# Kernel tuning notes

Measured on AMD Instinct MI355X. Metric: run time of the kernel, lower is better.

## Reference

```python
import jax, jax.numpy as jnp
import numpy as np

NEG_SLOPE = 0.01  # torch leaky_relu default

N_NODES = 100000
N_EDGES = 1600000
D = 64
N_BBOX = 4096


def setup_inputs() -> dict:
    key = jax.random.key(0)
    ks = jax.random.split(key, 9)
    x = jax.random.normal(ks[0], (N_NODES, D), dtype=jnp.float32)
    edge_index = jax.random.randint(ks[1], (2, N_EDGES), 0, N_NODES, dtype=jnp.int64)
    bbox = jax.random.randint(ks[2], (N_BBOX,), 0, N_NODES, dtype=jnp.int64)
    s = 1.0 / np.sqrt(D)
    W1_rel = jax.random.normal(ks[3], (D, D), dtype=jnp.float32) * s
    b1 = jax.random.normal(ks[4], (D,), dtype=jnp.float32) * s
    W1_root = jax.random.normal(ks[5], (D, D), dtype=jnp.float32) * s
    W2_rel = jax.random.normal(ks[6], (D, D), dtype=jnp.float32) * s
    b2 = jax.random.normal(ks[7], (D,), dtype=jnp.float32) * s
    W2_root = jax.random.normal(ks[8], (D, D), dtype=jnp.float32) * s
    return {"x": x, "edge_index": edge_index, "bbox": bbox,
            "W1_rel": W1_rel, "b1": b1, "W1_root": W1_root,
            "W2_rel": W2_rel, "b2": b2, "W2_root": W2_root}


def graph_conv(x, src, dst, W_rel, b, W_root):
    # PyG GraphConv: out_i = W_rel @ (sum_{j in N(i)} x_j) + b + W_root @ x_i
    msg = x[src]                                        # [E, D] gather
    agg = jax.ops.segment_sum(msg, dst, num_segments=x.shape[0])  # [N, D] scatter-add
    return agg @ W_rel + b + x @ W_root


def reference(x, edge_index, bbox, W1_rel, b1, W1_root, W2_rel, b2, W2_root):
    src, dst = edge_index[0], edge_index[1]
    h = graph_conv(x, src, dst, W1_rel, b1, W1_root)
    h = jax.nn.leaky_relu(h, NEG_SLOPE)
    # dropout is identity at inference (training=False)
    h = graph_conv(h, src, dst, W2_rel, b2, W2_root)
    h = jax.nn.leaky_relu(h, NEG_SLOPE)
    return h[bbox]
```

## Files before the change

### kernel.cpp

```cpp
#include <hip/hip_runtime.h>

#define N_NODES 100000
#define N_EDGES 1600000
#define D 64
#define N_BBOX 4096
#define CAP 64
#define NBITW 3136

typedef short bf16x8 __attribute__((ext_vector_type(8)));
typedef float f32x4 __attribute__((ext_vector_type(4)));

__device__ __forceinline__ float readlane_f(float v, int l) {
  return __int_as_float(__builtin_amdgcn_readlane(__float_as_int(v), l));
}
__device__ __forceinline__ int bperm(int srclane, int v) {
  return __builtin_amdgcn_ds_bpermute(srclane << 2, v);
}
__device__ __forceinline__ float lrelu(float v) {
  return fmaxf(v, 0.01f * v);
}
__device__ __forceinline__ bool testbit(const unsigned* bits, int i) {
  return (bits[i >> 5] >> (i & 31)) & 1u;
}
__device__ __forceinline__ short f2bf(float f) {
  unsigned u = __float_as_uint(f);
  u += 0x7FFFu + ((u >> 16) & 1u);
  return (short)(u >> 16);
}
__device__ __forceinline__ bf16x8 pack_bf8(float4 lo, float4 hi) {
  bf16x8 r;
  r[0] = f2bf(lo.x); r[1] = f2bf(lo.y); r[2] = f2bf(lo.z); r[3] = f2bf(lo.w);
  r[4] = f2bf(hi.x); r[5] = f2bf(hi.y); r[6] = f2bf(hi.z); r[7] = f2bf(hi.w);
  return r;
}

__global__ __launch_bounds__(256) void mark_kernel(const int* __restrict__ bbox,
                                                   unsigned* __restrict__ is_bbox_bits,
                                                   unsigned* __restrict__ needed_bits) {
  int t = blockIdx.x * blockDim.x + threadIdx.x;
  if (t < N_BBOX) {
    int n = bbox[t];
    unsigned m = 1u << (n & 31);
    atomicOr(&is_bbox_bits[n >> 5], m);
    atomicOr(&needed_bits[n >> 5], m);
  }
}

__global__ __launch_bounds__(256) void mark_needed_kernel(
    const int* __restrict__ src, const int* __restrict__ dst,
    const unsigned* __restrict__ is_bbox_bits, unsigned* __restrict__ needed_bits) {
  int e = blockIdx.x * blockDim.x + threadIdx.x;
  if (e >= N_EDGES) return;
  int d = dst[e];
  if (testbit(is_bbox_bits, d)) {
    int s = src[e];
    atomicOr(&needed_bits[s >> 5], 1u << (s & 31));
  }
}

__global__ __launch_bounds__(256) void fill_kernel(const int* __restrict__ src,
                                                   const int* __restrict__ dst,
                                                   const unsigned* __restrict__ needed_bits,
                                                   int* __restrict__ cnt,
                                                   int* __restrict__ slots) {
  int e = blockIdx.x * blockDim.x + threadIdx.x;
  if (e >= N_EDGES) return;
  int d = dst[e];
  if (!testbit(needed_bits, d)) return;
  int p = atomicAdd(&cnt[d], 1);
  if (p < CAP) slots[(size_t)d * CAP + p] = src[e];
}

__global__ __launch_bounds__(256) void gather1_kernel(const float4* __restrict__ x4,
                                                      const unsigned* __restrict__ needed_bits,
                                                      const int* __restrict__ cnt,
                                                      const int* __restrict__ slots,
                                                      float4* __restrict__ agg4) {
  const int wid = (blockIdx.x * blockDim.x + threadIdx.x) >> 6;
  if (wid >= N_NODES) return;
  if (!testbit(needed_bits, wid)) return;
  const int lane = threadIdx.x & 63;
  const int g = lane >> 4, c = lane & 15;

  int n = cnt[wid];
  n = (n > CAP) ? CAP : n;
  const int myslot = (lane < n) ? slots[(size_t)wid * CAP + lane] : 0;

  float4 acc = make_float4(0.f, 0.f, 0.f, 0.f);
  for (int e0 = 0; e0 < n; e0 += 32) {
    int idx[8], s[8];
    float4 v[8];
#pragma unroll
    for (int u = 0; u < 8; u++) {
      idx[u] = e0 + u * 4 + g;
      s[u] = bperm(idx[u], myslot);
    }
#pragma unroll
    for (int u = 0; u < 8; u++) {
      v[u] = make_float4(0.f, 0.f, 0.f, 0.f);
      if (idx[u] < n) v[u] = x4[(size_t)s[u] * 16 + c];
    }
#pragma unroll
    for (int u = 0; u < 8; u++) {
      acc.x += v[u].x; acc.y += v[u].y; acc.z += v[u].z; acc.w += v[u].w;
    }
  }
  acc.x += __shfl_xor(acc.x, 16); acc.y += __shfl_xor(acc.y, 16);
  acc.z += __shfl_xor(acc.z, 16); acc.w += __shfl_xor(acc.w, 16);
  acc.x += __shfl_xor(acc.x, 32); acc.y += __shfl_xor(acc.y, 32);
  acc.z += __shfl_xor(acc.z, 32); acc.w += __shfl_xor(acc.w, 32);
  if (g == 0) agg4[(size_t)wid * 16 + c] = acc;
}

__global__ __launch_bounds__(256, 1) void dense1_mfma_kernel(
    const float* __restrict__ x, const float* __restrict__ W1rel,
    const float* __restrict__ b1, const float* __restrict__ W1root,
    float* __restrict__ hbuf) {
  const int lane = threadIdx.x & 63;
  const int cn = lane & 15;
  const int quad = lane >> 4;
  const int wid0 = (blockIdx.x * blockDim.x + threadIdx.x) >> 6;
  const int nwaves = (gridDim.x * blockDim.x) >> 6;

  bf16x8 brel[2][4], broot[2][4];
#pragma unroll
  for (int kh = 0; kh < 2; kh++)
#pragma unroll
    for (int nt = 0; nt < 4; nt++)
#pragma unroll
      for (int i = 0; i < 8; i++) {
        const int k = kh * 32 + quad * 8 + i;
        brel[kh][nt][i] = f2bf(W1rel[k * D + nt * 16 + cn]);
        broot[kh][nt][i] = f2bf(W1root[k * D + nt * 16 + cn]);
      }
  float bj[4];
#pragma unroll
  for (int nt = 0; nt < 4; nt++) bj[nt] = b1[nt * 16 + cn];

  for (int tile = wid0; tile < N_NODES / 16; tile += nwaves) {
    const int node0 = tile * 16;
    const float* arow = hbuf + (size_t)(node0 + cn) * D;
    const float* xrow = x + (size_t)(node0 + cn) * D;

    f32x4 acc[4] = {};
#pragma unroll
    for (int kh = 0; kh < 2; kh++) {
      const int kb = kh * 32 + quad * 8;
      const float4 fa0 = *(const float4*)(arow + kb);
      const float4 fa1 = *(const float4*)(arow + kb + 4);
      const float4 fx0 = *(const float4*)(xrow + kb);
      const float4 fx1 = *(const float4*)(xrow + kb + 4);
      const bf16x8 a_agg = pack_bf8(fa0, fa1);
      const bf16x8 a_x = pack_bf8(fx0, fx1);
#pragma unroll
      for (int nt = 0; nt < 4; nt++) {
        acc[nt] = __builtin_amdgcn_mfma_f32_16x16x32_bf16(a_agg, brel[kh][nt],
                                                          acc[nt], 0, 0, 0);
        acc[nt] = __builtin_amdgcn_mfma_f32_16x16x32_bf16(a_x, broot[kh][nt],
                                                          acc[nt], 0, 0, 0);
      }
    }
#pragma unroll
    for (int nt = 0; nt < 4; nt++) {
#pragma unroll
      for (int r = 0; r < 4; r++) {
        const int row = quad * 4 + r;
        hbuf[(size_t)(node0 + row) * D + nt * 16 + cn] = lrelu(acc[nt][r] + bj[nt]);
      }
    }
  }
}

__global__ __launch_bounds__(256, 1) void layer2_kernel(
    const float4* __restrict__ h4, const int* __restrict__ cnt,
    const int* __restrict__ slots, const int* __restrict__ bbox,
    const float* __restrict__ W2rel, const float* __restrict__ b2,
    const float* __restrict__ W2root, float* __restrict__ out) {
  const int t = (blockIdx.x * blockDim.x + threadIdx.x) >> 6;
  if (t >= N_BBOX) return;
  const int lane = threadIdx.x & 63;
  const int g = lane >> 4, c = lane & 15;

  float wrel[D], wroot[D];
#pragma unroll
  for (int k = 0; k < D; k++) {
    wrel[k] = W2rel[k * D + lane];
    wroot[k] = W2root[k * D + lane];
  }
  const float bj = b2[lane];

  const int node = __builtin_amdgcn_readfirstlane(bbox[t]);
  int n = cnt[node];
  n = (n > CAP) ? CAP : n;
  const int myslot = (lane < n) ? slots[(size_t)node * CAP + lane] : 0;

  float4 acc = make_float4(0.f, 0.f, 0.f, 0.f);
  for (int e0 = 0; e0 < n; e0 += 32) {
    int idx[8], s[8];
    float4 v[8];
#pragma unroll
    for (int u = 0; u < 8; u++) {
      idx[u] = e0 + u * 4 + g;
      s[u] = bperm(idx[u], myslot);
    }
#pragma unroll
    for (int u = 0; u < 8; u++) {
      v[u] = make_float4(0.f, 0.f, 0.f, 0.f);
      if (idx[u] < n) v[u] = h4[(size_t)s[u] * 16 + c];
    }
#pragma unroll
    for (int u = 0; u < 8; u++) {
      acc.x += v[u].x; acc.y += v[u].y; acc.z += v[u].z; acc.w += v[u].w;
    }
  }
  acc.x += __shfl_xor(acc.x, 16); acc.y += __shfl_xor(acc.y, 16);
  acc.z += __shfl_xor(acc.z, 16); acc.w += __shfl_xor(acc.w, 16);
  acc.x += __shfl_xor(acc.x, 32); acc.y += __shfl_xor(acc.y, 32);
  acc.z += __shfl_xor(acc.z, 32); acc.w += __shfl_xor(acc.w, 32);

  const float hi = ((const float*)h4)[(size_t)node * D + lane];
  float s0 = 0.f, s1 = 0.f, s2 = 0.f, s3 = 0.f;
#pragma unroll
  for (int k = 0; k < D; k += 2) {
    const float a0 = (k & 2) ? readlane_f(acc.z, k >> 2) : readlane_f(acc.x, k >> 2);
    const float a1 = ((k + 1) & 2) ? readlane_f(acc.w, (k + 1) >> 2)
                                   : readlane_f(acc.y, (k + 1) >> 2);
    s0 += a0 * wrel[k];
    s1 += readlane_f(hi, k) * wroot[k];
    s2 += a1 * wrel[k + 1];
    s3 += readlane_f(hi, k + 1) * wroot[k + 1];
  }
  out[(size_t)t * D + lane] = lrelu(bj + ((s0 + s1) + (s2 + s3)));
}


extern "C" void kernel_launch(void* const* d_in, const int* in_sizes, int n_in,
                              void* d_out, int out_size, void* d_ws, size_t ws_size,
                              hipStream_t stream) {
  const float* x = (const float*)d_in[0];
  const int* ei = (const int*)d_in[1];
  const int* src = ei;
  const int* dst = ei + N_EDGES;
  const int* bbox = (const int*)d_in[2];
  const float* W1rel = (const float*)d_in[3];
  const float* b1 = (const float*)d_in[4];
  const float* W1root = (const float*)d_in[5];
  const float* W2rel = (const float*)d_in[6];
  const float* b2 = (const float*)d_in[7];
  const float* W2root = (const float*)d_in[8];
  float* out = (float*)d_out;

  char* ws = (char*)d_ws;
  size_t off = 0;
  auto alloc = [&](size_t bytes) -> char* {
    char* p = ws + off;
    off = (off + bytes + 511) & ~(size_t)511;
    return p;
  };
  unsigned* is_bbox_bits = (unsigned*)alloc(NBITW * sizeof(unsigned));
  unsigned* needed_bits = (unsigned*)alloc(NBITW * sizeof(unsigned));
  int* cnt = (int*)alloc(N_NODES * sizeof(int));
  char* zero_end = ws + off;
  int* slots = (int*)alloc((size_t)N_NODES * CAP * sizeof(int));
  float* hbuf = (float*)alloc((size_t)N_NODES * D * sizeof(float));

  hipMemsetAsync(is_bbox_bits, 0, (size_t)(zero_end - (char*)is_bbox_bits), stream);
  mark_kernel<<<(N_BBOX + 255) / 256, 256, 0, stream>>>(bbox, is_bbox_bits,
                                                        needed_bits);
  mark_needed_kernel<<<(N_EDGES + 255) / 256, 256, 0, stream>>>(
      src, dst, is_bbox_bits, needed_bits);
  fill_kernel<<<(N_EDGES + 255) / 256, 256, 0, stream>>>(src, dst, needed_bits,
                                                         cnt, slots);
  gather1_kernel<<<(N_NODES + 3) / 4, 256, 0, stream>>>(
      (const float4*)x, needed_bits, cnt, slots, (float4*)hbuf);
  dense1_mfma_kernel<<<512, 256, 0, stream>>>(x, W1rel, b1, W1root, hbuf);
  layer2_kernel<<<(N_BBOX + 3) / 4, 256, 0, stream>>>(
      (const float4*)hbuf, cnt, slots, bbox, W2rel, b2, W2root, out);
}
```

Measured before the change: 201.7 us.

## Fuse layer-1 gather and dense MFMA through LDS, skip unneeded nodes

Merges the neighbor-aggregation kernel and the dense MFMA kernel into one kernel. Each block aggregates 64 nodes into LDS, then runs bf16 MFMA directly from LDS, so the aggregate no longer round-trips through global memory. hbuf is now written only for nodes layer 2 needs. A small prep kernel pre-transposes and converts the weights to bf16 so each block loads them with vector reads instead of converting scalars itself. The risks are lower occupancy from launch_bounds(256,1) plus LDS use, and serialized per-wave gather loops of 16 nodes each.

```diff
diff --git a/kernel.cpp b/kernel.cpp
--- a/kernel.cpp
+++ b/kernel.cpp
@@ -6,6 +6,7 @@
 #define N_BBOX 4096
 #define CAP 64
 #define NBITW 3136
+#define NTILE 1563
 
 typedef short bf16x8 __attribute__((ext_vector_type(8)));
 typedef float f32x4 __attribute__((ext_vector_type(4)));
@@ -71,102 +72,107 @@
   if (p < CAP) slots[(size_t)d * CAP + p] = src[e];
 }
 
-__global__ __launch_bounds__(256) void gather1_kernel(const float4* __restrict__ x4,
-                                                      const unsigned* __restrict__ needed_bits,
-                                                      const int* __restrict__ cnt,
-                                                      const int* __restrict__ slots,
-                                                      float4* __restrict__ agg4) {
-  const int wid = (blockIdx.x * blockDim.x + threadIdx.x) >> 6;
-  if (wid >= N_NODES) return;
-  if (!testbit(needed_bits, wid)) return;
+__global__ __launch_bounds__(256) void wprep_kernel(const float* __restrict__ W1rel,
+                                                    const float* __restrict__ W1root,
+                                                    short* __restrict__ wrelT,
+                                                    short* __restrict__ wrootT) {
+  int i = blockIdx.x * blockDim.x + threadIdx.x;
+  if (i < D * D) {
+    int n = i >> 6, k = i & 63;
+    wrelT[n * D + k] = f2bf(W1rel[k * D + n]);
+    wrootT[n * D + k] = f2bf(W1root[k * D + n]);
+  }
+}
+
+__global__ __launch_bounds__(256, 1) void layer1_fused_kernel(
+    const float4* __restrict__ x4, const unsigned* __restrict__ needed_bits,
+    const int* __restrict__ cnt, const int* __restrict__ slots,
+    const short* __restrict__ wrelT, const short* __restrict__ wrootT,
+    const float* __restrict__ b1, float* __restrict__ hbuf) {
+  __shared__ float lds[64 * 68];
   const int lane = threadIdx.x & 63;
+  const int w = threadIdx.x >> 6;
   const int g = lane >> 4, c = lane & 15;
 
-  int n = cnt[wid];
-  n = (n > CAP) ? CAP : n;
-  const int myslot = (lane < n) ? slots[(size_t)wid * CAP + lane] : 0;
-
-  float4 acc = make_float4(0.f, 0.f, 0.f, 0.f);
-  for (int e0 = 0; e0 < n; e0 += 32) {
-    int idx[8], s[8];
-    float4 v[8];
-#pragma unroll
-    for (int u = 0; u < 8; u++) {
-      idx[u] = e0 + u * 4 + g;
-      s[u] = bperm(idx[u], myslot);
-    }
-#pragma unroll
-    for (int u = 0; u < 8; u++) {
-      v[u] = make_float4(0.f, 0.f, 0.f, 0.f);
-      if (idx[u] < n) v[u] = x4[(size_t)s[u] * 16 + c];
-    }
-#pragma unroll
-    for (int u = 0; u < 8; u++) {
-      acc.x += v[u].x; acc.y += v[u].y; acc.z += v[u].z; acc.w += v[u].w;
-    }
-  }
-  acc.x += __shfl_xor(acc.x, 16); acc.y += __shfl_xor(acc.y, 16);
-  acc.z += __shfl_xor(acc.z, 16); acc.w += __shfl_xor(acc.w, 16);
-  acc.x += __shfl_xor(acc.x, 32); acc.y += __shfl_xor(acc.y, 32);
-  acc.z += __shfl_xor(acc.z, 32); acc.w += __shfl_xor(acc.w, 32);
-  if (g == 0) agg4[(size_t)wid * 16 + c] = acc;
-}
-
-__global__ __launch_bounds__(256, 1) void dense1_mfma_kernel(
-    const float* __restrict__ x, const float* __restrict__ W1rel,
-    const float* __restrict__ b1, const float* __restrict__ W1root,
-    float* __restrict__ hbuf) {
-  const int lane = threadIdx.x & 63;
-  const int cn = lane & 15;
-  const int quad = lane >> 4;
-  const int wid0 = (blockIdx.x * blockDim.x + threadIdx.x) >> 6;
-  const int nwaves = (gridDim.x * blockDim.x) >> 6;
-
   bf16x8 brel[2][4], broot[2][4];
 #pragma unroll
   for (int kh = 0; kh < 2; kh++)
 #pragma unroll
-    for (int nt = 0; nt < 4; nt++)
-#pragma unroll
-      for (int i = 0; i < 8; i++) {
-        const int k = kh * 32 + quad * 8 + i;
-        brel[kh][nt][i] = f2bf(W1rel[k * D + nt * 16 + cn]);
-        broot[kh][nt][i] = f2bf(W1root[k * D + nt * 16 + cn]);
+    for (int nt = 0; nt < 4; nt++) {
+      const int nn = nt * 16 + c;
+      const int kb = kh * 32 + g * 8;
+      brel[kh][nt] = *(const bf16x8*)&wrelT[nn * D + kb];
+      broot[kh][nt] = *(const bf16x8*)&wrootT[nn * D + kb];
+    }
+  float bj[4];
+#pragma unroll
+  for (int nt = 0; nt < 4; nt++) bj[nt] = b1[nt * 16 + c];
+
+  const int node0 = blockIdx.x * 64 + w * 16;
+
+  for (int li = 0; li < 16; li++) {
+    const int node = node0 + li;
+    if (node >= N_NODES) break;
+    if (!testbit(needed_bits, node)) continue;
+    int n = cnt[node];
+    n = (n > CAP) ? CAP : n;
+    const int myslot = (lane < n) ? slots[(size_t)node * CAP + lane] : 0;
+
+    float4 acc = make_float4(0.f, 0.f, 0.f, 0.f);
+    for (int e0 = 0; e0 < n; e0 += 32) {
+      int idx[8], s[8];
+      float4 v[8];
+#pragma unroll
+      for (int u = 0; u < 8; u++) {
+        idx[u] = e0 + u * 4 + g;
+        s[u] = bperm(idx[u], myslot);
       }
-  float bj[4];
-#pragma unroll
-  for (int nt = 0; nt < 4; nt++) bj[nt] = b1[nt * 16 + cn];
-
-  for (int tile = wid0; tile < N_NODES / 16; tile += nwaves) {
-    const int node0 = tile * 16;
-    const float* arow = hbuf + (size_t)(node0 + cn) * D;
-    const float* xrow = x + (size_t)(node0 + cn) * D;
-
-    f32x4 acc[4] = {};
-#pragma unroll
-    for (int kh = 0; kh < 2; kh++) {
-      const int kb = kh * 32 + quad * 8;
-      const float4 fa0 = *(const float4*)(arow + kb);
-      const float4 fa1 = *(const float4*)(arow + kb + 4);
-      const float4 fx0 = *(const float4*)(xrow + kb);
-      const float4 fx1 = *(const float4*)(xrow + kb + 4);
-      const bf16x8 a_agg = pack_bf8(fa0, fa1);
-      const bf16x8 a_x = pack_bf8(fx0, fx1);
-#pragma unroll
-      for (int nt = 0; nt < 4; nt++) {
-        acc[nt] = __builtin_amdgcn_mfma_f32_16x16x32_bf16(a_agg, brel[kh][nt],
-                                                          acc[nt], 0, 0, 0);
-        acc[nt] = __builtin_amdgcn_mfma_f32_16x16x32_bf16(a_x, broot[kh][nt],
-                                                          acc[nt], 0, 0, 0);
+#pragma unroll
+      for (int u = 0; u < 8; u++) {
+        v[u] = make_float4(0.f, 0.f, 0.f, 0.f);
+        if (idx[u] < n) v[u] = x4[(size_t)s[u] * 16 + c];
       }
-    }
+#pragma unroll
+      for (int u = 0; u < 8; u++) {
+        acc.x += v[u].x; acc.y += v[u].y; acc.z += v[u].z; acc.w += v[u].w;
+      }
+    }
+    acc.x += __shfl_xor(acc.x, 16); acc.y += __shfl_xor(acc.y, 16);
+    acc.z += __shfl_xor(acc.z, 16); acc.w += __shfl_xor(acc.w, 16);
+    acc.x += __shfl_xor(acc.x, 32); acc.y += __shfl_xor(acc.y, 32);
+    acc.z += __shfl_xor(acc.z, 32); acc.w += __shfl_xor(acc.w, 32);
+    if (g == 0) *(float4*)&lds[(w * 16 + li) * 68 + 4 * c] = acc;
+  }
+  __syncthreads();
+
+  f32x4 acc2[4] = {};
+  const int arow_base = (w * 16 + c) * 68;
+  const int xnode = (node0 + c < N_NODES) ? node0 + c : N_NODES - 1;
+  const float* xrow = (const float*)x4 + (size_t)xnode * D;
+#pragma unroll
+  for (int kh = 0; kh < 2; kh++) {
+    const int kb = kh * 32 + g * 8;
+    const float4 fa0 = *(const float4*)&lds[arow_base + kb];
+    const float4 fa1 = *(const float4*)&lds[arow_base + kb + 4];
+    const float4 fx0 = *(const float4*)(xrow + kb);
+    const float4 fx1 = *(const float4*)(xrow + kb + 4);
+    const bf16x8 a_agg = pack_bf8(fa0, fa1);
+    const bf16x8 a_x = pack_bf8(fx0, fx1);
 #pragma unroll
     for (int nt = 0; nt < 4; nt++) {
-#pragma unroll
-      for (int r = 0; r < 4; r++) {
-        const int row = quad * 4 + r;
-        hbuf[(size_t)(node0 + row) * D + nt * 16 + cn] = lrelu(acc[nt][r] + bj[nt]);
-      }
+      acc2[nt] = __builtin_amdgcn_mfma_f32_16x16x32_bf16(a_agg, brel[kh][nt],
+                                                         acc2[nt], 0, 0, 0);
+      acc2[nt] = __builtin_amdgcn_mfma_f32_16x16x32_bf16(a_x, broot[kh][nt],
+                                                         acc2[nt], 0, 0, 0);
+    }
+  }
+#pragma unroll
+  for (int r = 0; r < 4; r++) {
+    const int node = node0 + g * 4 + r;
+    if (node < N_NODES && testbit(needed_bits, node)) {
+#pragma unroll
+      for (int nt = 0; nt < 4; nt++)
+        hbuf[(size_t)node * D + nt * 16 + c] = lrelu(acc2[nt][r] + bj[nt]);
     }
   }
 }
@@ -263,6 +269,8 @@
   char* zero_end = ws + off;
   int* slots = (int*)alloc((size_t)N_NODES * CAP * sizeof(int));
   float* hbuf = (float*)alloc((size_t)N_NODES * D * sizeof(float));
+  short* wrelT = (short*)alloc(D * D * sizeof(short));
+  short* wrootT = (short*)alloc(D * D * sizeof(short));
 
   hipMemsetAsync(is_bbox_bits, 0, (size_t)(zero_end - (char*)is_bbox_bits), stream);
   mark_kernel<<<(N_BBOX + 255) / 256, 256, 0, stream>>>(bbox, is_bbox_bits,
@@ -271,9 +279,10 @@
       src, dst, is_bbox_bits, needed_bits);
   fill_kernel<<<(N_EDGES + 255) / 256, 256, 0, stream>>>(src, dst, needed_bits,
                                                          cnt, slots);
-  gather1_kernel<<<(N_NODES + 3) / 4, 256, 0, stream>>>(
-      (const float4*)x, needed_bits, cnt, slots, (float4*)hbuf);
-  dense1_mfma_kernel<<<512, 256, 0, stream>>>(x, W1rel, b1, W1root, hbuf);
+  wprep_kernel<<<(D * D + 255) / 256, 256, 0, stream>>>(W1rel, W1root, wrelT,
+                                                        wrootT);
+  layer1_fused_kernel<<<NTILE, 256, 0, stream>>>(
+      (const float4*)x, needed_bits, cnt, slots, wrelT, wrootT, b1, hbuf);
   layer2_kernel<<<(N_BBOX + 3) / 4, 256, 0, stream>>>(
       (const float4*)hbuf, cnt, slots, bbox, W2rel, b2, W2root, out);
 }
```

New measurement: 225.2 us. 11.7% more time.

## Partition fill kernel by destination range across block groups with vectorized edge reads

Applied to the files above, without the earlier changes.

The fill kernel now launches a fixed 1024-block grid split into 8 groups. Each group owns one slice of destination node IDs and grid-strides over all edges, reading dst as int4. Only edges whose destination falls in the group's slice and is marked needed do atomic increments and slot writes. The aim is to keep each group's cnt/slots atomics and writes on a smaller, more cache-local region, perhaps aligned with XCDs. The cost is that the dst array is read 8 times.

```diff
diff --git a/kernel.cpp b/kernel.cpp
--- a/kernel.cpp
+++ b/kernel.cpp
@@ -6,6 +6,7 @@
 #define N_BBOX 4096
 #define CAP 64
 #define NBITW 3136
+#define SLICE 12500
 
 typedef short bf16x8 __attribute__((ext_vector_type(8)));
 typedef float f32x4 __attribute__((ext_vector_type(4)));
@@ -58,17 +59,38 @@
   }
 }
 
-__global__ __launch_bounds__(256) void fill_kernel(const int* __restrict__ src,
-                                                   const int* __restrict__ dst,
+__global__ __launch_bounds__(256) void fill_kernel(const int4* __restrict__ src4,
+                                                   const int4* __restrict__ dst4,
                                                    const unsigned* __restrict__ needed_bits,
                                                    int* __restrict__ cnt,
                                                    int* __restrict__ slots) {
-  int e = blockIdx.x * blockDim.x + threadIdx.x;
-  if (e >= N_EDGES) return;
-  int d = dst[e];
-  if (!testbit(needed_bits, d)) return;
-  int p = atomicAdd(&cnt[d], 1);
-  if (p < CAP) slots[(size_t)d * CAP + p] = src[e];
+  const int grp = blockIdx.x & 7;
+  const int bidx = blockIdx.x >> 3;
+  const int nblk = gridDim.x >> 3;
+  const int lo = grp * SLICE;
+  const int hi = lo + SLICE;
+  const int nq = N_EDGES / 4;
+
+  for (int q = bidx * blockDim.x + threadIdx.x; q < nq; q += nblk * blockDim.x) {
+    const int4 d4 = dst4[q];
+    const int dd[4] = {d4.x, d4.y, d4.z, d4.w};
+    bool m[4], any = false;
+#pragma unroll
+    for (int u = 0; u < 4; u++) {
+      m[u] = (dd[u] >= lo) & (dd[u] < hi);
+      if (m[u]) m[u] = testbit(needed_bits, dd[u]);
+      any |= m[u];
+    }
+    if (!any) continue;
+    const int4 s4 = src4[q];
+    const int ss[4] = {s4.x, s4.y, s4.z, s4.w};
+#pragma unroll
+    for (int u = 0; u < 4; u++) {
+      if (!m[u]) continue;
+      int p = atomicAdd(&cnt[dd[u]], 1);
+      if (p < CAP) slots[(size_t)dd[u] * CAP + p] = ss[u];
+    }
+  }
 }
 
 __global__ __launch_bounds__(256) void gather1_kernel(const float4* __restrict__ x4,
@@ -269,8 +291,8 @@
                                                         needed_bits);
   mark_needed_kernel<<<(N_EDGES + 255) / 256, 256, 0, stream>>>(
       src, dst, is_bbox_bits, needed_bits);
-  fill_kernel<<<(N_EDGES + 255) / 256, 256, 0, stream>>>(src, dst, needed_bits,
-                                                         cnt, slots);
+  fill_kernel<<<1024, 256, 0, stream>>>((const int4*)src, (const int4*)dst,
+                                        needed_bits, cnt, slots);
   gather1_kernel<<<(N_NODES + 3) / 4, 256, 0, stream>>>(
       (const float4*)x, needed_bits, cnt, slots, (float4*)hbuf);
   dense1_mfma_kernel<<<512, 256, 0, stream>>>(x, W1rel, b1, W1root, hbuf);
```

Result: slower. 206.2 us (+2.2%).
